# Performance work log

Hardware: AMD Instinct MI355X
Metric: run time of the kernel (lower is better)

## Reference

```python
import jax, jax.numpy as jnp
import numpy as np

B, S, D, H, FF, L = 2, 2048, 512, 8, 2048, 2
HD = D // H
EPS = 1e-5
NEG = -1e9


def layernorm(x, gamma, beta):
    # mean/var over last axis (axis=2 in original)
    mean = jnp.mean(x, axis=-1, keepdims=True)
    var = jnp.mean((x - mean) ** 2, axis=-1, keepdims=True)
    return gamma * (x - mean) / jnp.sqrt(var + EPS) + beta


def masked_attention(x, mask, Wqkv, Wo, bo):
    b, s, d = x.shape
    qkv = x @ Wqkv                                  # [B,S,3D]
    qkv = qkv.reshape(b, s, H, 3 * HD)
    qkv = qkv.reshape(b, H, s, 3 * HD)              # original uses reshape, not transpose
    q, k, v = jnp.split(qkv, 3, axis=3)             # each [B,H,S,HD]
    scaled = jnp.einsum('bhqd,bhkd->bhqk', q, k) / (HD ** 0.5)
    col = mask[:, None, None, :]                    # valid key columns
    row = mask[:, None, :, None]                    # valid query rows
    logits = jnp.where(col, scaled, NEG)
    attn = jax.nn.softmax(logits, axis=-1)
    attn = attn * (row & col).astype(attn.dtype)    # exact zeros outside valid block
    values = jnp.einsum('bhqk,bhkd->bhqd', attn, v)  # [B,H,S,HD]
    values = values.reshape(b, s, H * HD)           # original uses reshape, not transpose
    return values @ Wo + bo


def encoder_layer(x, mask, p):
    res = x
    x = masked_attention(x, mask, p['Wqkv'], p['Wo'], p['bo'])
    x = layernorm(x + res, p['g1'], p['be1'])
    res = x
    x = jax.nn.relu(x @ p['W1'] + p['bf1']) @ p['W2'] + p['bf2']
    x = layernorm(x + res, p['g2'], p['be2'])
    return x


def setup_inputs() -> dict:
    key = jax.random.key(0)
    ks = jax.random.split(key, 8)
    x = jax.random.normal(ks[0], (B, S, D), jnp.float32)
    lengths = jax.random.randint(ks[1], (B,), S // 2, S + 1)
    paded_mask = jnp.arange(S)[None, :] < lengths[:, None]   # [B,S] bool
    sc = 0.02
    return {
        'x': x,
        'paded_mask': paded_mask,
        'Wqkv': jax.random.normal(ks[2], (L, D, 3 * D), jnp.float32) * sc,
        'Wo': jax.random.normal(ks[3], (L, D, D), jnp.float32) * sc,
        'bo': jnp.zeros((L, D), jnp.float32),
        'g1': jnp.ones((L, D), jnp.float32),
        'be1': jnp.zeros((L, D), jnp.float32),
        'W1': jax.random.normal(ks[4], (L, D, FF), jnp.float32) * sc,
        'bf1': jnp.zeros((L, FF), jnp.float32),
        'W2': jax.random.normal(ks[5], (L, FF, D), jnp.float32) * sc,
        'bf2': jnp.zeros((L, D), jnp.float32),
        'g2': jnp.ones((L, D), jnp.float32),
        'be2': jnp.zeros((L, D), jnp.float32),
    }


def reference(x, paded_mask, Wqkv, Wo, bo, g1, be1, W1, bf1, W2, bf2, g2, be2):
    for i in range(L):
        p = {'Wqkv': Wqkv[i], 'Wo': Wo[i], 'bo': bo[i], 'g1': g1[i], 'be1': be1[i],
             'W1': W1[i], 'bf1': bf1[i], 'W2': W2[i], 'bf2': bf2[i], 'g2': g2[i], 'be2': be2[i]}
        x = encoder_layer(x, paded_mask, p)
    return x
```

## Files before the change

### kernel.cpp

```cpp
#include <hip/hip_runtime.h>
#include <math.h>


typedef __bf16 bf16x8 __attribute__((ext_vector_type(8)));
typedef __bf16 bf16x4 __attribute__((ext_vector_type(4)));
typedef float f32x4 __attribute__((ext_vector_type(4)));

static constexpr int S_ = 2048;
static constexpr int D_ = 512;
static constexpr int FF_ = 2048;
static constexpr int M_ = 4096;

#define GLDS16(gp, lp)                                                      \
  __builtin_amdgcn_global_load_lds(                                         \
      (const __attribute__((address_space(1))) void*)(gp),                  \
      (__attribute__((address_space(3))) void*)(lp), 16, 0, 0)

__global__ __launch_bounds__(256) void prep_kernel(
    const float* __restrict__ Wqkv, const float* __restrict__ Wo,
    const float* __restrict__ W1, const float* __restrict__ W2,
    const float* __restrict__ x,
    __bf16* __restrict__ WqkvT, __bf16* __restrict__ WoT,
    __bf16* __restrict__ W1T, __bf16* __restrict__ W2T,
    __bf16* __restrict__ x_bf) {
  __shared__ float tile[32][33];
  const int t = threadIdx.x;
  int bid = blockIdx.x;
  if (bid >= 6144) {
    const size_t i = ((size_t)(bid - 6144) * 256 + t) * 8;
    float4 f0 = *(const float4*)(x + i), f1 = *(const float4*)(x + i + 4);
    bf16x8 v;
    v[0] = (__bf16)f0.x; v[1] = (__bf16)f0.y; v[2] = (__bf16)f0.z; v[3] = (__bf16)f0.w;
    v[4] = (__bf16)f1.x; v[5] = (__bf16)f1.y; v[6] = (__bf16)f1.z; v[7] = (__bf16)f1.w;
    *(bf16x8*)(x_bf + i) = v;
    return;
  }
  const float* W;
  __bf16* Wt;
  int K, N;
  if (bid < 1536)      { W = Wqkv;              Wt = WqkvT; K = 512;  N = 1536; }
  else if (bid < 2048) { bid -= 1536; W = Wo;   Wt = WoT;   K = 512;  N = 512; }
  else if (bid < 4096) { bid -= 2048; W = W1;   Wt = W1T;   K = 512;  N = 2048; }
  else                 { bid -= 4096; W = W2;   Wt = W2T;   K = 2048; N = 512; }
  const int nx = N >> 5, ny = K >> 5;
  const int xb = bid % nx, yb = (bid / nx) % ny, l = bid / (nx * ny);
  const size_t off = (size_t)l * K * N;
  const int n0 = xb * 32, k0 = yb * 32;
  const int tx = t & 31, ty = t >> 5;
#pragma unroll
  for (int i = 0; i < 4; ++i)
    tile[ty + i * 8][tx] = W[off + (size_t)(k0 + ty + i * 8) * N + n0 + tx];
  __syncthreads();
#pragma unroll
  for (int i = 0; i < 4; ++i)
    Wt[off + (size_t)(n0 + ty + i * 8) * K + k0 + tx] = (__bf16)tile[tx][ty + i * 8];
}

template <int BN, bool RELU, bool SPLITK2, bool QKV, bool OUT_BF16>
__global__ __launch_bounds__(256) void gemm_async(
    const __bf16* __restrict__ A, const __bf16* __restrict__ Wt,
    const float* __restrict__ bias, void* __restrict__ Cv,
    __bf16* __restrict__ VT, int M, int N, int K) {
  constexpr int BM = 128, BK = 64;
  constexpr int MI = 4;
  constexpr int NJ = BN / 32;
  __shared__ __bf16 As[BM][BK];
  __shared__ __bf16 Bs[BN][BK];

  const int t = threadIdx.x;
  const int wv = t >> 6, ln = t & 63;
  const int ln16 = t & 15, quad = (t & 63) >> 4;
  const int bm = blockIdx.x * BM, bn = blockIdx.y * BN;
  const int wm = (wv & 1) * 64, wn = (wv >> 1) * (BN / 2);

  int kbeg = 0, kend = K;
  if (SPLITK2) {
    const int half = K >> 1;
    kbeg = blockIdx.z * half;
    kend = kbeg + half;
  }

  f32x4 acc[MI][NJ];
#pragma unroll
  for (int i = 0; i < MI; ++i)
#pragma unroll
    for (int j = 0; j < NJ; ++j) acc[i][j] = {0.f, 0.f, 0.f, 0.f};

  for (int k0 = kbeg; k0 < kend; k0 += BK) {
#pragma unroll
    for (int it = 0; it < 4; ++it) {
      const int cb = it * 256 + wv * 64;
      const int c = cb + ln;
      const int r = c >> 3, jl = (c & 7) ^ (r & 7);
      GLDS16(A + (size_t)(bm + r) * K + k0 + jl * 8,
             (char*)&As[0][0] + (size_t)cb * 16);
    }
#pragma unroll
    for (int it = 0; it < BN / 32; ++it) {
      const int cb = it * 256 + wv * 64;
      const int c = cb + ln;
      const int r = c >> 3, jl = (c & 7) ^ (r & 7);
      GLDS16(Wt + (size_t)(bn + r) * K + k0 + jl * 8,
             (char*)&Bs[0][0] + (size_t)cb * 16);
    }
    __syncthreads();

#pragma unroll
    for (int kk = 0; kk < 2; ++kk) {
      bf16x8 a[MI], b[NJ];
#pragma unroll
      for (int i = 0; i < MI; ++i) {
        const int r = wm + i * 16 + ln16;
        a[i] = *(const bf16x8*)&As[r][((kk * 4 + quad) ^ (r & 7)) * 8];
      }
#pragma unroll
      for (int j = 0; j < NJ; ++j) {
        const int r = wn + j * 16 + ln16;
        b[j] = *(const bf16x8*)&Bs[r][((kk * 4 + quad) ^ (r & 7)) * 8];
      }
#pragma unroll
      for (int i = 0; i < MI; ++i)
#pragma unroll
        for (int j = 0; j < NJ; ++j)
          acc[i][j] = __builtin_amdgcn_mfma_f32_16x16x32_bf16(a[i], b[j], acc[i][j], 0, 0, 0);
    }
    __syncthreads();
  }

  float* Cs = (float*)Cv;
  if (SPLITK2) Cs += (size_t)blockIdx.z * M * N;
  const bool addb = bias && (!SPLITK2 || blockIdx.z == 0);
  const int bidx = bm >> 11;
#pragma unroll
  for (int i = 0; i < MI; ++i) {
#pragma unroll
    for (int j = 0; j < NJ; ++j) {
      const int col = bn + wn + j * 16 + ln16;
      if (QKV && (col % 192) >= 128) {
        const int d = col % 192 - 128;
        const int n8 = col / 192;
#pragma unroll
        for (int r = 0; r < 4; ++r) {
          const int s = (bm + wm + i * 16 + quad * 4 + r) & 2047;
          const int h = s >> 8;
          const int s2 = ((s & 255) << 3) | n8;
          VT[(((size_t)(bidx * 8 + h) * 64 + d) << 11) + s2] = (__bf16)acc[i][j][r];
        }
      } else {
        const float bv = addb ? bias[col] : 0.f;
#pragma unroll
        for (int r = 0; r < 4; ++r) {
          const int row = bm + wm + i * 16 + quad * 4 + r;
          float v = acc[i][j][r] + bv;
          if (RELU) v = fmaxf(v, 0.f);
          if (OUT_BF16)
            ((__bf16*)Cv)[(size_t)row * N + col] = (__bf16)v;
          else
            Cs[(size_t)row * N + col] = v;
        }
      }
    }
  }
}

__global__ __launch_bounds__(512) void attn_mfma(
    const __bf16* __restrict__ qkv, const __bf16* __restrict__ VT,
    const int* __restrict__ mask, __bf16* __restrict__ O) {
  const int b = blockIdx.z;
  const int h = blockIdx.y;
  const int q0 = blockIdx.x * 64;
  const int t = threadIdx.x;
  const int g = t >> 8;
  const int tl = t & 255;
  const int wq = tl >> 6;
  const int ln16 = t & 15, quad = (t & 63) >> 4;

  __shared__ __bf16 Ks[2][64][64];
  __shared__ __bf16 Vt[2][64][72];
  __shared__ __bf16 Ps[2][64][64];
  __shared__ int lred[4];
  __shared__ int len_sh;

  const __bf16* base = qkv + (size_t)b * S_ * 1536 + (size_t)h * S_ * 192;
  const __bf16* vbase = VT + ((size_t)(b * 8 + h) << 17);
  __bf16* obase = O + (size_t)b * S_ * 512 + h * 64;

  if (t < 256) {
    int c = 0;
    const int* mp = mask + b * S_ + t * 8;
#pragma unroll
    for (int i = 0; i < 8; ++i) c += mp[i];
#pragma unroll
    for (int off = 32; off >= 1; off >>= 1) c += __shfl_down(c, off, 64);
    if ((t & 63) == 0) lred[t >> 6] = c;
  }
  __syncthreads();
  if (t == 0) len_sh = lred[0] + lred[1] + lred[2] + lred[3];
  __syncthreads();
  const int len = len_sh;

  if (q0 >= len) {
    const int r = t >> 3, c = (t & 7) * 8;
    bf16x8 z = {};
    *(bf16x8*)(obase + (size_t)(q0 + r) * 512 + c) = z;
    return;
  }

  bf16x8 aq[2];
  {
    const int q = q0 + wq * 16 + ln16;
    aq[0] = *(const bf16x8*)(base + (size_t)q * 192 + quad * 8);
    aq[1] = *(const bf16x8*)(base + (size_t)q * 192 + 32 + quad * 8);
  }

  float lpart = 0.f;
  f32x4 o[4];
#pragma unroll
  for (int d = 0; d < 4; ++d) o[d] = {0.f, 0.f, 0.f, 0.f};

  const int kr = tl >> 3;
  const int kcs = ((tl & 7) ^ (kr & 7)) * 8;
  const int vd = tl >> 2, vc = (tl & 3) * 16;
  const int vphys = vc ^ ((vd & 3) * 16);
  const int srow = wq * 16 + ln16;
  const int sswz = ln16 & 7;

  bf16x8 kreg[2], vreg[2];
  auto fetch = [&](int kt) {
    kreg[0] = *(const bf16x8*)(base + (size_t)(kt + kr) * 192 + 64 + ((tl & 7) * 8));
    kreg[1] = *(const bf16x8*)(base + (size_t)(kt + kr + 32) * 192 + 64 + ((tl & 7) * 8));
    const __bf16* vp = vbase + (size_t)vd * 2048 + kt + vc;
    vreg[0] = *(const bf16x8*)vp;
    vreg[1] = *(const bf16x8*)(vp + 8);
  };

  fetch(g * 64);

  const int nit = (len + 127) >> 7;
  for (int i = 0; i < nit; ++i) {
    const int k0 = g * 64 + i * 128;
    *(bf16x8*)&Ks[g][kr][kcs] = kreg[0];
    *(bf16x8*)&Ks[g][kr + 32][kcs] = kreg[1];
    *(bf16x8*)&Vt[g][vd][vphys] = vreg[0];
    *(bf16x8*)&Vt[g][vd][vphys + 8] = vreg[1];
    __syncthreads();

    {
      int kp = k0 + 128;
      if (kp > S_ - 64) kp = k0;
      fetch(kp);
    }

    f32x4 sf[4];
#pragma unroll
    for (int j = 0; j < 4; ++j) sf[j] = {0.f, 0.f, 0.f, 0.f};
    __builtin_amdgcn_s_setprio(1);
#pragma unroll
    for (int kk = 0; kk < 2; ++kk) {
#pragma unroll
      for (int j = 0; j < 4; ++j) {
        bf16x8 ak = *(const bf16x8*)&Ks[g][j * 16 + ln16][((kk * 4 + quad) ^ sswz) * 8];
        sf[j] = __builtin_amdgcn_mfma_f32_16x16x32_bf16(ak, aq[kk], sf[j], 0, 0, 0);
      }
    }
    __builtin_amdgcn_s_setprio(0);

    if (k0 + 64 <= len) {
#pragma unroll
      for (int j = 0; j < 4; ++j) {
        bf16x4 pk;
#pragma unroll
        for (int r = 0; r < 4; ++r) {
          const float p = exp2f(fminf(sf[j][r] * 0.18033688f, 86.5617f));
          lpart += p;
          pk[r] = (__bf16)p;
        }
        const int pg = ((j * 2 + (quad >> 1)) ^ sswz) * 8 + (quad & 1) * 4;
        *(bf16x4*)&Ps[g][srow][pg] = pk;
      }
    } else {
#pragma unroll
      for (int j = 0; j < 4; ++j) {
        bf16x4 pk;
#pragma unroll
        for (int r = 0; r < 4; ++r) {
          const float e = exp2f(fminf(sf[j][r] * 0.18033688f, 86.5617f));
          const float p = (k0 + j * 16 + quad * 4 + r < len) ? e : 0.f;
          lpart += p;
          pk[r] = (__bf16)p;
        }
        const int pg = ((j * 2 + (quad >> 1)) ^ sswz) * 8 + (quad & 1) * 4;
        *(bf16x4*)&Ps[g][srow][pg] = pk;
      }
    }
    asm volatile("s_waitcnt lgkmcnt(0)" ::: "memory");

    __builtin_amdgcn_s_setprio(1);
#pragma unroll
    for (int kk = 0; kk < 2; ++kk) {
      bf16x8 pb = *(const bf16x8*)&Ps[g][srow][((kk * 4 + quad) ^ sswz) * 8];
#pragma unroll
      for (int dt = 0; dt < 4; ++dt) {
        bf16x8 av = *(const bf16x8*)
            &Vt[g][dt * 16 + ln16][(kk * 32 + quad * 8) ^ ((ln16 & 3) * 16)];
        o[dt] = __builtin_amdgcn_mfma_f32_16x16x32_bf16(av, pb, o[dt], 0, 0, 0);
      }
    }
    __builtin_amdgcn_s_setprio(0);
    __syncthreads();
  }

  lpart += __shfl_xor(lpart, 16, 64);
  lpart += __shfl_xor(lpart, 32, 64);

  float* obuf = (float*)&Ks[0][0][0];
  float* lbuf = (float*)&Vt[0][0][0];
  const int row = srow;
  if (g == 1) {
#pragma unroll
    for (int dt = 0; dt < 4; ++dt)
      *(f32x4*)&obuf[row * 64 + dt * 16 + quad * 4] = o[dt];
    if (quad == 0) lbuf[row] = lpart;
  }
  __syncthreads();
  if (g == 0) {
    const int q = q0 + row;
    const float l = lpart + lbuf[row];
    const float s = (q < len) ? 1.f / l : 0.f;
#pragma unroll
    for (int dt = 0; dt < 4; ++dt) {
      const f32x4 o1 = *(const f32x4*)&obuf[row * 64 + dt * 16 + quad * 4];
      bf16x4 ov;
#pragma unroll
      for (int r = 0; r < 4; ++r) ov[r] = (__bf16)((o[dt][r] + o1[r]) * s);
      *(bf16x4*)(obase + (size_t)q * 512 + dt * 16 + quad * 4) = ov;
    }
  }
}

__global__ __launch_bounds__(256) void add_ln_kernel(
    const float* __restrict__ a, const float* __restrict__ a2,
    const float* __restrict__ res, const float* __restrict__ g,
    const float* __restrict__ be, float* __restrict__ out,
    __bf16* __restrict__ out_bf) {
  const int row = blockIdx.x * 4 + (threadIdx.x >> 6);
  const int ln = threadIdx.x & 63;
  const int c = ln * 8;
  const float* pa = a + (size_t)row * D_ + c;
  const float* pr = res + (size_t)row * D_ + c;

  float4 v0 = *(const float4*)pa, v1 = *(const float4*)(pa + 4);
  float4 r0 = *(const float4*)pr, r1 = *(const float4*)(pr + 4);
  float w[8] = {v0.x + r0.x, v0.y + r0.y, v0.z + r0.z, v0.w + r0.w,
                v1.x + r1.x, v1.y + r1.y, v1.z + r1.z, v1.w + r1.w};
  if (a2) {
    const float* p2 = a2 + (size_t)row * D_ + c;
    float4 u0 = *(const float4*)p2, u1 = *(const float4*)(p2 + 4);
    w[0] += u0.x; w[1] += u0.y; w[2] += u0.z; w[3] += u0.w;
    w[4] += u1.x; w[5] += u1.y; w[6] += u1.z; w[7] += u1.w;
  }
  float s = 0.f, sq = 0.f;
#pragma unroll
  for (int e = 0; e < 8; ++e) {
    s += w[e];
    sq += w[e] * w[e];
  }
#pragma unroll
  for (int off = 1; off < 64; off <<= 1) {
    s += __shfl_xor(s, off, 64);
    sq += __shfl_xor(sq, off, 64);
  }
  const float mean = s * (1.0f / D_);
  const float var = sq * (1.0f / D_) - mean * mean;
  const float rstd = rsqrtf(var + 1e-5f);

  float4 g0 = *(const float4*)(g + c), g1 = *(const float4*)(g + c + 4);
  float4 b0 = *(const float4*)(be + c), b1 = *(const float4*)(be + c + 4);
  const float gv[8] = {g0.x, g0.y, g0.z, g0.w, g1.x, g1.y, g1.z, g1.w};
  const float bv[8] = {b0.x, b0.y, b0.z, b0.w, b1.x, b1.y, b1.z, b1.w};
  float y[8];
#pragma unroll
  for (int e = 0; e < 8; ++e) y[e] = gv[e] * (w[e] - mean) * rstd + bv[e];

  float* po = out + (size_t)row * D_ + c;
  *(float4*)po = make_float4(y[0], y[1], y[2], y[3]);
  *(float4*)(po + 4) = make_float4(y[4], y[5], y[6], y[7]);
  if (out_bf) {
    bf16x8 v;
#pragma unroll
    for (int e = 0; e < 8; ++e) v[e] = (__bf16)y[e];
    *(bf16x8*)(out_bf + (size_t)row * D_ + c) = v;
  }
}

extern "C" void kernel_launch(void* const* d_in, const int* in_sizes, int n_in,
                              void* d_out, int out_size, void* d_ws, size_t ws_size,
                              hipStream_t stream) {
  const float* x_in = (const float*)d_in[0];
  const int* mask   = (const int*)d_in[1];
  const float* Wqkv = (const float*)d_in[2];
  const float* Wo   = (const float*)d_in[3];
  const float* bo   = (const float*)d_in[4];
  const float* g1   = (const float*)d_in[5];
  const float* be1  = (const float*)d_in[6];
  const float* W1   = (const float*)d_in[7];
  const float* bf1  = (const float*)d_in[8];
  const float* W2   = (const float*)d_in[9];
  const float* bf2  = (const float*)d_in[10];
  const float* g2   = (const float*)d_in[11];
  const float* be2  = (const float*)d_in[12];
  float* out = (float*)d_out;

  char* w = (char*)d_ws;
  auto alloc = [&](size_t bytes) {
    char* p = w;
    w += (bytes + 255) & ~(size_t)255;
    return p;
  };
  __bf16* WqkvT = (__bf16*)alloc((size_t)2 * 512 * 1536 * 2);
  __bf16* WoT   = (__bf16*)alloc((size_t)2 * 512 * 512 * 2);
  __bf16* W1T   = (__bf16*)alloc((size_t)2 * 512 * 2048 * 2);
  __bf16* W2T   = (__bf16*)alloc((size_t)2 * 2048 * 512 * 2);
  __bf16* R1    = (__bf16*)alloc((size_t)M_ * FF_ * 2);
  __bf16* VTb   = (__bf16*)alloc((size_t)16 * 64 * 2048 * 2);
  float* R2     = (float*)alloc((size_t)2 * M_ * D_ * 4);
  __bf16* Obf   = (__bf16*)alloc((size_t)M_ * D_ * 2);
  float* proj   = (float*)alloc((size_t)M_ * D_ * 4);
  float* x1     = (float*)alloc((size_t)M_ * D_ * 4);
  float* xE     = (float*)alloc((size_t)M_ * D_ * 4);
  __bf16* x_bf  = (__bf16*)alloc((size_t)M_ * D_ * 2);
  __bf16* x1_bf = (__bf16*)alloc((size_t)M_ * D_ * 2);
  __bf16* xE_bf = (__bf16*)alloc((size_t)M_ * D_ * 2);

  prep_kernel<<<dim3(7168), 256, 0, stream>>>(Wqkv, Wo, W1, W2, x_in,
                                              WqkvT, WoT, W1T, W2T, x_bf);

  for (int l = 0; l < 2; ++l) {
    const float* xin = (l == 0) ? x_in : xE;
    const __bf16* xin_bf = (l == 0) ? x_bf : xE_bf;
    float* xout = (l == 1) ? out : xE;
    __bf16* xout_bf = (l == 0) ? xE_bf : nullptr;
    const __bf16* WqkvT_l = WqkvT + (size_t)l * 512 * 1536;
    const __bf16* WoT_l   = WoT + (size_t)l * 512 * 512;
    const __bf16* W1T_l   = W1T + (size_t)l * 512 * 2048;
    const __bf16* W2T_l   = W2T + (size_t)l * 2048 * 512;

    gemm_async<64, false, false, true, true><<<dim3(32, 24), 256, 0, stream>>>(
        xin_bf, WqkvT_l, nullptr, R1, VTb, M_, 1536, 512);
    attn_mfma<<<dim3(S_ / 64, 8, 2), 512, 0, stream>>>(R1, VTb, mask, Obf);
    gemm_async<64, false, false, false, false><<<dim3(32, 8), 256, 0, stream>>>(
        Obf, WoT_l, bo + (size_t)l * D_, proj, nullptr, M_, 512, 512);
    add_ln_kernel<<<dim3(M_ / 4), 256, 0, stream>>>(proj, nullptr, xin,
                                                    g1 + (size_t)l * D_,
                                                    be1 + (size_t)l * D_, x1, x1_bf);
    gemm_async<128, true, false, false, true><<<dim3(32, 16), 256, 0, stream>>>(
        x1_bf, W1T_l, bf1 + (size_t)l * FF_, R1, nullptr, M_, 2048, 512);
    gemm_async<64, false, true, false, false><<<dim3(32, 8, 2), 256, 0, stream>>>(
        R1, W2T_l, bf2 + (size_t)l * D_, R2, nullptr, M_, 512, 2048);
    add_ln_kernel<<<dim3(M_ / 4), 256, 0, stream>>>(R2, R2 + (size_t)M_ * D_, x1,
                                                    g2 + (size_t)l * D_,
                                                    be2 + (size_t)l * D_, xout, xout_bf);
  }
}
```

Before: 339.9 us.

## Precompute mask lengths, fold softmax scale into Q, double-buffer K tiles in attention

The per-batch valid lengths are now computed once in the prep kernel, so the attention kernel no longer reduces the mask or pays two barriers per block. The softmax scale (including log2e) is applied to Q in the QKV GEMM epilogue, which removes a multiply per score. K tiles are double-buffered in shared memory and prefetched two iterations ahead, with the barrier moved from the loop top to between the score and PV phases. A launch-bounds occupancy hint is also added. In exchange, shared memory grows, and scaling Q before the bf16 rounding slightly changes precision.

Result: no change. 345.8 us (+1.7%).

```diff
diff --git a/kernel.cpp b/kernel.cpp
--- a/kernel.cpp
+++ b/kernel.cpp
@@ -19,13 +19,25 @@
 __global__ __launch_bounds__(256) void prep_kernel(
     const float* __restrict__ Wqkv, const float* __restrict__ Wo,
     const float* __restrict__ W1, const float* __restrict__ W2,
-    const float* __restrict__ x,
+    const float* __restrict__ x, const int* __restrict__ mask,
     __bf16* __restrict__ WqkvT, __bf16* __restrict__ WoT,
     __bf16* __restrict__ W1T, __bf16* __restrict__ W2T,
-    __bf16* __restrict__ x_bf) {
+    __bf16* __restrict__ x_bf, int* __restrict__ lens) {
   __shared__ float tile[32][33];
   const int t = threadIdx.x;
   int bid = blockIdx.x;
+  if (bid == 7168) {
+    if (t < 128) {
+      const int b = t >> 6, ln = t & 63;
+      int c = 0;
+#pragma unroll
+      for (int i = 0; i < 32; ++i) c += mask[b * S_ + ln * 32 + i];
+#pragma unroll
+      for (int off = 32; off >= 1; off >>= 1) c += __shfl_down(c, off, 64);
+      if (ln == 0) lens[b] = c;
+    }
+    return;
+  }
   if (bid >= 6144) {
     const size_t i = ((size_t)(bid - 6144) * 256 + t) * 8;
     float4 f0 = *(const float4*)(x + i), f1 = *(const float4*)(x + i + 4);
@@ -148,11 +160,13 @@
         }
       } else {
         const float bv = addb ? bias[col] : 0.f;
+        const bool isQ = QKV && (col % 192) < 64;
 #pragma unroll
         for (int r = 0; r < 4; ++r) {
           const int row = bm + wm + i * 16 + quad * 4 + r;
           float v = acc[i][j][r] + bv;
           if (RELU) v = fmaxf(v, 0.f);
+          if (isQ) v *= 0.18033688f;
           if (OUT_BF16)
             ((__bf16*)Cv)[(size_t)row * N + col] = (__bf16)v;
           else
@@ -163,9 +177,9 @@
   }
 }
 
-__global__ __launch_bounds__(512) void attn_mfma(
+__global__ __launch_bounds__(512, 4) void attn_mfma(
     const __bf16* __restrict__ qkv, const __bf16* __restrict__ VT,
-    const int* __restrict__ mask, __bf16* __restrict__ O) {
+    const int* __restrict__ lens, __bf16* __restrict__ O) {
   const int b = blockIdx.z;
   const int h = blockIdx.y;
   const int q0 = blockIdx.x * 64;
@@ -175,29 +189,14 @@
   const int wq = tl >> 6;
   const int ln16 = t & 15, quad = (t & 63) >> 4;
 
-  __shared__ __bf16 Ks[2][64][64];
+  __shared__ __bf16 Ks[2][2][64][64];
   __shared__ __bf16 Vt[2][64][72];
   __shared__ __bf16 Ps[2][64][64];
-  __shared__ int lred[4];
-  __shared__ int len_sh;
-
+
+  const int len = lens[b];
   const __bf16* base = qkv + (size_t)b * S_ * 1536 + (size_t)h * S_ * 192;
   const __bf16* vbase = VT + ((size_t)(b * 8 + h) << 17);
   __bf16* obase = O + (size_t)b * S_ * 512 + h * 64;
-
-  if (t < 256) {
-    int c = 0;
-    const int* mp = mask + b * S_ + t * 8;
-#pragma unroll
-    for (int i = 0; i < 8; ++i) c += mp[i];
-#pragma unroll
-    for (int off = 32; off >= 1; off >>= 1) c += __shfl_down(c, off, 64);
-    if ((t & 63) == 0) lred[t >> 6] = c;
-  }
-  __syncthreads();
-  if (t == 0) len_sh = lred[0] + lred[1] + lred[2] + lred[3];
-  __syncthreads();
-  const int len = len_sh;
 
   if (q0 >= len) {
     const int r = t >> 3, c = (t & 7) * 8;
@@ -226,29 +225,45 @@
   const int sswz = ln16 & 7;
 
   bf16x8 kreg[2], vreg[2];
-  auto fetch = [&](int kt) {
-    kreg[0] = *(const bf16x8*)(base + (size_t)(kt + kr) * 192 + 64 + ((tl & 7) * 8));
-    kreg[1] = *(const bf16x8*)(base + (size_t)(kt + kr + 32) * 192 + 64 + ((tl & 7) * 8));
+  auto fetchK = [&](int kt) {
+    kreg[0] = *(const bf16x8*)(base + (size_t)(kt + kr) * 192 + 64 + (tl & 7) * 8);
+    kreg[1] = *(const bf16x8*)(base + (size_t)(kt + kr + 32) * 192 + 64 + (tl & 7) * 8);
+  };
+  auto fetchV = [&](int kt) {
     const __bf16* vp = vbase + (size_t)vd * 2048 + kt + vc;
     vreg[0] = *(const bf16x8*)vp;
     vreg[1] = *(const bf16x8*)(vp + 8);
   };
 
-  fetch(g * 64);
-
   const int nit = (len + 127) >> 7;
+
+  fetchK(g * 64);
+  fetchV(g * 64);
+  *(bf16x8*)&Ks[0][g][kr][kcs] = kreg[0];
+  *(bf16x8*)&Ks[0][g][kr + 32][kcs] = kreg[1];
+  {
+    int kp = g * 64 + 128;
+    if (kp > S_ - 64) kp = g * 64;
+    fetchK(kp);
+  }
+  __syncthreads();
+
+  int buf = 0;
   for (int i = 0; i < nit; ++i) {
     const int k0 = g * 64 + i * 128;
-    *(bf16x8*)&Ks[g][kr][kcs] = kreg[0];
-    *(bf16x8*)&Ks[g][kr + 32][kcs] = kreg[1];
     *(bf16x8*)&Vt[g][vd][vphys] = vreg[0];
     *(bf16x8*)&Vt[g][vd][vphys + 8] = vreg[1];
-    __syncthreads();
-
+    *(bf16x8*)&Ks[buf ^ 1][g][kr][kcs] = kreg[0];
+    *(bf16x8*)&Ks[buf ^ 1][g][kr + 32][kcs] = kreg[1];
+    {
+      int kp = k0 + 256;
+      if (kp > S_ - 64) kp = k0;
+      fetchK(kp);
+    }
     {
       int kp = k0 + 128;
       if (kp > S_ - 64) kp = k0;
-      fetch(kp);
+      fetchV(kp);
     }
 
     f32x4 sf[4];
@@ -259,7 +274,7 @@
     for (int kk = 0; kk < 2; ++kk) {
 #pragma unroll
       for (int j = 0; j < 4; ++j) {
-        bf16x8 ak = *(const bf16x8*)&Ks[g][j * 16 + ln16][((kk * 4 + quad) ^ sswz) * 8];
+        bf16x8 ak = *(const bf16x8*)&Ks[buf][g][j * 16 + ln16][((kk * 4 + quad) ^ sswz) * 8];
         sf[j] = __builtin_amdgcn_mfma_f32_16x16x32_bf16(ak, aq[kk], sf[j], 0, 0, 0);
       }
     }
@@ -271,7 +286,7 @@
         bf16x4 pk;
 #pragma unroll
         for (int r = 0; r < 4; ++r) {
-          const float p = exp2f(fminf(sf[j][r] * 0.18033688f, 86.5617f));
+          const float p = exp2f(fminf(sf[j][r], 86.5617f));
           lpart += p;
           pk[r] = (__bf16)p;
         }
@@ -284,7 +299,7 @@
         bf16x4 pk;
 #pragma unroll
         for (int r = 0; r < 4; ++r) {
-          const float e = exp2f(fminf(sf[j][r] * 0.18033688f, 86.5617f));
+          const float e = exp2f(fminf(sf[j][r], 86.5617f));
           const float p = (k0 + j * 16 + quad * 4 + r < len) ? e : 0.f;
           lpart += p;
           pk[r] = (__bf16)p;
@@ -293,7 +308,8 @@
         *(bf16x4*)&Ps[g][srow][pg] = pk;
       }
     }
-    asm volatile("s_waitcnt lgkmcnt(0)" ::: "memory");
+
+    __syncthreads();
 
     __builtin_amdgcn_s_setprio(1);
 #pragma unroll
@@ -308,13 +324,14 @@
     }
     __builtin_amdgcn_s_setprio(0);
     __syncthreads();
+    buf ^= 1;
   }
 
   lpart += __shfl_xor(lpart, 16, 64);
   lpart += __shfl_xor(lpart, 32, 64);
 
-  float* obuf = (float*)&Ks[0][0][0];
-  float* lbuf = (float*)&Vt[0][0][0];
+  float* obuf = (float*)&Ks[0][0][0][0];
+  float* lbuf = (float*)&Ps[0][0][0];
   const int row = srow;
   if (g == 1) {
 #pragma unroll
@@ -428,12 +445,13 @@
   float* proj   = (float*)alloc((size_t)M_ * D_ * 4);
   float* x1     = (float*)alloc((size_t)M_ * D_ * 4);
   float* xE     = (float*)alloc((size_t)M_ * D_ * 4);
+  int*   lens   = (int*)alloc(256);
   __bf16* x_bf  = (__bf16*)alloc((size_t)M_ * D_ * 2);
   __bf16* x1_bf = (__bf16*)alloc((size_t)M_ * D_ * 2);
   __bf16* xE_bf = (__bf16*)alloc((size_t)M_ * D_ * 2);
 
-  prep_kernel<<<dim3(7168), 256, 0, stream>>>(Wqkv, Wo, W1, W2, x_in,
-                                              WqkvT, WoT, W1T, W2T, x_bf);
+  prep_kernel<<<dim3(7169), 256, 0, stream>>>(Wqkv, Wo, W1, W2, x_in, mask,
+                                              WqkvT, WoT, W1T, W2T, x_bf, lens);
 
   for (int l = 0; l < 2; ++l) {
     const float* xin = (l == 0) ? x_in : xE;
@@ -447,7 +465,7 @@
 
     gemm_async<64, false, false, true, true><<<dim3(32, 24), 256, 0, stream>>>(
         xin_bf, WqkvT_l, nullptr, R1, VTb, M_, 1536, 512);
-    attn_mfma<<<dim3(S_ / 64, 8, 2), 512, 0, stream>>>(R1, VTb, mask, Obf);
+    attn_mfma<<<dim3(S_ / 64, 8, 2), 512, 0, stream>>>(R1, VTb, lens, Obf);
     gemm_async<64, false, false, false, false><<<dim3(32, 8), 256, 0, stream>>>(
         Obf, WoT_l, bo + (size_t)l * D_, proj, nullptr, M_, 512, 512);
     add_ln_kernel<<<dim3(M_ / 4), 256, 0, stream>>>(proj, nullptr, xin,
```
